# Kernel optimization log

Hardware: AMD Instinct MI355X
Metric: run time of the kernel (lower is better)

## Reference

```python
import jax, jax.numpy as jnp
import numpy as np
import math

NHEAD = 16
FACTOR = 5


def setup_inputs() -> dict:
    key = jax.random.key(0)
    ks = jax.random.split(key, 10)
    B, L, Dm = 2, 2048, 1024
    x = jax.random.normal(ks[0], (B, L, Dm), dtype=jnp.float32)
    w = lambda k: jax.random.normal(k, (Dm, Dm), dtype=jnp.float32) * 0.02
    b = lambda k: jax.random.normal(k, (Dm,), dtype=jnp.float32) * 0.02
    return {
        "x": x,
        "Wq": w(ks[1]), "bq": b(ks[2]),
        "Wk": w(ks[3]), "bk": b(ks[4]),
        "Wv": w(ks[5]), "bv": b(ks[6]),
        "Wo": w(ks[7]), "bo": b(ks[8]),
    }


def reference(x, Wq, bq, Wk, bk, Wv, bv, Wo, bo):
    B, L, Dm = x.shape
    H = NHEAD
    D = Dm // H
    # U = number of top scores kept per query row (ProbSparse sparsity level)
    U = min(L, int(FACTOR * math.log(L)) if L > 1 else L)

    def proj(W, b):
        # torch Linear: x @ W^T + b ; then [B,L,H,D] -> [B,H,L,D]
        return (x @ W.T + b).reshape(B, L, H, D).transpose(0, 2, 1, 3)

    Q = proj(Wq, bq)
    K = proj(Wk, bk)
    V = proj(Wv, bv)

    scores = jnp.einsum("bhqd,bhkd->bhqk", Q, K) / math.sqrt(D)  # [B,H,L,L]
    # kth-largest score per row; keep entries >= threshold (ties kept, matching torch semantics)
    thresh = jax.lax.top_k(scores, U)[0][..., -1:]  # [B,H,L,1]
    scores = jnp.where(scores < thresh, -jnp.inf, scores)
    attn = jax.nn.softmax(scores, axis=-1)  # dropout is identity in eval
    context = jnp.einsum("bhqk,bhkd->bhqd", attn, V)
    context = context.transpose(0, 2, 1, 3).reshape(B, L, Dm)
    return context @ Wo.T + bo
```

## Files before the change

### kernel.cpp

```cpp
#include <hip/hip_runtime.h>
#include <math.h>

#define BB 2
#define LL 2048
#define DM 1024
#define NH 16
#define HD 64

__device__ __forceinline__ unsigned mono32(float f) {
    unsigned u = __float_as_uint(f);
    return (u & 0x80000000u) ? ~u : (u | 0x80000000u);
}
__device__ __forceinline__ float unmono32(unsigned m) {
    const unsigned u = (m & 0x80000000u) ? (m & 0x7FFFFFFFu) : ~m;
    return __uint_as_float(u);
}

__global__ __launch_bounds__(256) void transpose1024(
    const float* __restrict__ in, float* __restrict__ out)
{
    __shared__ float t[32][33];
    const int bx = blockIdx.x * 32, by = blockIdx.y * 32;
    const int tx = threadIdx.x & 31, ty = threadIdx.x >> 5;
    for (int r = ty; r < 32; r += 8)
        t[r][tx] = in[(size_t)(by + r) * DM + bx + tx];
    __syncthreads();
    for (int r = ty; r < 32; r += 8)
        out[(size_t)(bx + r) * DM + by + tx] = t[tx][r];
}

__global__ __launch_bounds__(256) void proj_emul(
    const float* __restrict__ x, const float* __restrict__ Wt,
    const float* __restrict__ bias, float* __restrict__ outp)
{
    __shared__ float xs[8][DM];
    const int tid = threadIdx.x;
    const int n4  = tid * 4;
    const int m0  = blockIdx.x * 8;

    for (int i = tid; i < 8 * 256; i += 256) {
        const int r = i >> 8, c4 = (i & 255) << 2;
        *(float4*)&xs[r][c4] = *(const float4*)&x[(size_t)(m0 + r) * DM + c4];
    }
    __syncthreads();

    const int kbound[4] = {0, 384, 704, 1024};

    float S[8][4] = {};
#pragma unroll
    for (int p = 0; p < 3; p++) {
        float P[8][4] = {};
        for (int k = kbound[p]; k < kbound[p + 1]; k += 4) {
            const float4 w0 = *(const float4*)&Wt[(size_t)(k + 0) * DM + n4];
            const float4 w1 = *(const float4*)&Wt[(size_t)(k + 1) * DM + n4];
            const float4 w2 = *(const float4*)&Wt[(size_t)(k + 2) * DM + n4];
            const float4 w3 = *(const float4*)&Wt[(size_t)(k + 3) * DM + n4];
#pragma unroll
            for (int m = 0; m < 8; m++) {
                const float4 xv = *(const float4*)&xs[m][k];
                P[m][0] = fmaf(xv.x, w0.x, P[m][0]);
                P[m][1] = fmaf(xv.x, w0.y, P[m][1]);
                P[m][2] = fmaf(xv.x, w0.z, P[m][2]);
                P[m][3] = fmaf(xv.x, w0.w, P[m][3]);
                P[m][0] = fmaf(xv.y, w1.x, P[m][0]);
                P[m][1] = fmaf(xv.y, w1.y, P[m][1]);
                P[m][2] = fmaf(xv.y, w1.z, P[m][2]);
                P[m][3] = fmaf(xv.y, w1.w, P[m][3]);
                P[m][0] = fmaf(xv.z, w2.x, P[m][0]);
                P[m][1] = fmaf(xv.z, w2.y, P[m][1]);
                P[m][2] = fmaf(xv.z, w2.z, P[m][2]);
                P[m][3] = fmaf(xv.z, w2.w, P[m][3]);
                P[m][0] = fmaf(xv.w, w3.x, P[m][0]);
                P[m][1] = fmaf(xv.w, w3.y, P[m][1]);
                P[m][2] = fmaf(xv.w, w3.z, P[m][2]);
                P[m][3] = fmaf(xv.w, w3.w, P[m][3]);
            }
        }
#pragma unroll
        for (int m = 0; m < 8; m++) {
#pragma unroll
            for (int j = 0; j < 4; j++) S[m][j] += P[m][j];
        }
    }

    const float4 b4v = *(const float4*)&bias[n4];
    const int h = n4 / HD, d0 = n4 % HD;
#pragma unroll
    for (int m = 0; m < 8; m++) {
        const int mm = m0 + m;
        const int b = mm / LL, l = mm % LL;
        float4 o;
        o.x = S[m][0] + b4v.x; o.y = S[m][1] + b4v.y;
        o.z = S[m][2] + b4v.z; o.w = S[m][3] + b4v.w;
        *(float4*)&outp[(((size_t)b * NH + h) * LL + l) * HD + d0] = o;
    }
}

template <int MODE>
__global__ __launch_bounds__(256) void gemm_f32(
    const float* __restrict__ A, const float* __restrict__ W,
    const float* __restrict__ bias, float* __restrict__ out,
    int M, int N, int K)
{
    __shared__ float As[16][64];
    __shared__ float Bs[16][64];
    const int tid = threadIdx.x;
    const int m0 = blockIdx.y * 64;
    const int n0 = blockIdx.x * 64;
    const int tx = tid & 15, ty = tid >> 4;
    const int lr = tid >> 2, lc = (tid & 3) * 4;

    float acc[4][4] = {};

    for (int k0 = 0; k0 < K; k0 += 16) {
        float4 a4 = *(const float4*)&A[(size_t)(m0 + lr) * K + k0 + lc];
        float4 b4 = *(const float4*)&W[(size_t)(n0 + lr) * K + k0 + lc];
        __syncthreads();
        As[lc + 0][lr] = a4.x; As[lc + 1][lr] = a4.y;
        As[lc + 2][lr] = a4.z; As[lc + 3][lr] = a4.w;
        Bs[lc + 0][lr] = b4.x; Bs[lc + 1][lr] = b4.y;
        Bs[lc + 2][lr] = b4.z; Bs[lc + 3][lr] = b4.w;
        __syncthreads();
#pragma unroll
        for (int kk = 0; kk < 16; kk++) {
            float4 av = *(const float4*)&As[kk][ty * 4];
            float4 bv = *(const float4*)&Bs[kk][tx * 4];
            float a[4] = {av.x, av.y, av.z, av.w};
            float b[4] = {bv.x, bv.y, bv.z, bv.w};
#pragma unroll
            for (int i = 0; i < 4; i++)
#pragma unroll
                for (int j = 0; j < 4; j++)
                    acc[i][j] = fmaf(a[i], b[j], acc[i][j]);
        }
    }

#pragma unroll
    for (int i = 0; i < 4; i++) {
        const int m = m0 + ty * 4 + i;
#pragma unroll
        for (int j = 0; j < 4; j++) {
            const int n = n0 + tx * 4 + j;
            const float v = acc[i][j] + bias[n];
            if (MODE == 0) {
                const int b = m / LL, l = m % LL;
                const int h = n / HD, d = n % HD;
                out[(((size_t)b * NH + h) * LL + l) * HD + d] = v;
            } else {
                out[(size_t)m * N + n] = v;
            }
        }
    }
}

__global__ __launch_bounds__(256) void score_np(
    const float* __restrict__ Qf, const float* __restrict__ Kf,
    unsigned* __restrict__ scw, int bh0)
{
#pragma clang fp contract(off)
    const int tid  = threadIdx.x;
    const int lane = tid & 63;
    const int wv   = tid >> 6;
    const int l0   = blockIdx.x * 16;
    const int bhl  = blockIdx.y;
    const int bh   = bh0 + bhl;

    __shared__ float kt[256][68];
    __shared__ float qsh[16][64];

    const float* __restrict__ Kb = Kf + (size_t)bh * LL * HD;

    {
        const int r = tid >> 4, d4q = tid & 15;
        *(float4*)&qsh[r][d4q * 4] =
            *(const float4*)&Qf[((size_t)bh * LL + l0 + r) * HD + d4q * 4];
    }

    const int r0 = wv * 4;
    unsigned* __restrict__ s0 = scw + ((size_t)bhl * LL + l0 + r0 + 0) * LL;
    unsigned* __restrict__ s1 = scw + ((size_t)bhl * LL + l0 + r0 + 1) * LL;
    unsigned* __restrict__ s2 = scw + ((size_t)bhl * LL + l0 + r0 + 2) * LL;
    unsigned* __restrict__ s3 = scw + ((size_t)bhl * LL + l0 + r0 + 3) * LL;

    for (int kp = 0; kp < 8; kp++) {
        __syncthreads();
        {
            const float* src = Kb + ((size_t)kp * 256 + tid) * HD;
#pragma unroll
            for (int i = 0; i < 16; i++)
                *(float4*)&kt[tid][i * 4] = *(const float4*)&src[i * 4];
        }
        __syncthreads();

        float4 acc[4][4];
#pragma unroll
        for (int r = 0; r < 4; r++)
#pragma unroll
            for (int j = 0; j < 4; j++)
                acc[r][j] = make_float4(0.f, 0.f, 0.f, 0.f);

#pragma unroll
        for (int t = 0; t < 4; t++) {
#pragma unroll
            for (int sub = 3; sub >= 0; sub--) {
                const int d4 = 4 * t + sub;
                float4 kf0 = *(const float4*)&kt[0 * 64 + lane][d4 * 4];
                float4 kf1 = *(const float4*)&kt[1 * 64 + lane][d4 * 4];
                float4 kf2 = *(const float4*)&kt[2 * 64 + lane][d4 * 4];
                float4 kf3 = *(const float4*)&kt[3 * 64 + lane][d4 * 4];
                float4 qv0 = *(const float4*)&qsh[r0 + 0][d4 * 4];
                float4 qv1 = *(const float4*)&qsh[r0 + 1][d4 * 4];
                float4 qv2 = *(const float4*)&qsh[r0 + 2][d4 * 4];
                float4 qv3 = *(const float4*)&qsh[r0 + 3][d4 * 4];
#pragma unroll
                for (int r = 0; r < 4; r++) {
                    const float4 q = (r == 0) ? qv0 : (r == 1) ? qv1
                                   : (r == 2) ? qv2 : qv3;
#pragma unroll
                    for (int j = 0; j < 4; j++) {
                        const float4 k = (j == 0) ? kf0 : (j == 1) ? kf1
                                       : (j == 2) ? kf2 : kf3;
                        acc[r][j].x = q.x * k.x + acc[r][j].x;
                        acc[r][j].y = q.y * k.y + acc[r][j].y;
                        acc[r][j].z = q.z * k.z + acc[r][j].z;
                        acc[r][j].w = q.w * k.w + acc[r][j].w;
                    }
                }
            }
        }

#pragma unroll
        for (int j = 0; j < 4; j++) {
            const int kk = kp * 256 + j * 64 + lane;
            s0[kk] = mono32(((acc[0][j].x + acc[0][j].y) +
                             (acc[0][j].z + acc[0][j].w)) * 0.125f);
            s1[kk] = mono32(((acc[1][j].x + acc[1][j].y) +
                             (acc[1][j].z + acc[1][j].w)) * 0.125f);
            s2[kk] = mono32(((acc[2][j].x + acc[2][j].y) +
                             (acc[2][j].z + acc[2][j].w)) * 0.125f);
            s3[kk] = mono32(((acc[3][j].x + acc[3][j].y) +
                             (acc[3][j].z + acc[3][j].w)) * 0.125f);
        }
    }
}

__global__ __launch_bounds__(256) void select_np(
    const unsigned* __restrict__ scw, const float* __restrict__ Vf,
    float* __restrict__ ctx, int U, int bh0)
{
#pragma clang fp contract(off)
    const int tid  = threadIdx.x;
    const int lane = tid & 63;
    const int wv   = tid >> 6;
    const int l0   = blockIdx.x * 8;
    const int bhl  = blockIdx.y;
    const int bh   = bh0 + bhl;
    const int b    = bh / NH;
    const int h    = bh % NH;

    __shared__ float wls[8][64];
    __shared__ int   kls[8][64];

    const unsigned long long laneLT = (1ull << lane) - 1ull;
    const float* __restrict__ Vb = Vf + (size_t)bh * LL * HD;

#pragma unroll
    for (int rr8 = 0; rr8 < 2; rr8++) {
        const int rr = wv * 2 + rr8;
        const unsigned* __restrict__ srow =
            scw + ((size_t)bhl * LL + l0 + rr) * LL;

        unsigned mv[32];
#pragma unroll
        for (int j = 0; j < 32; j++) mv[j] = srow[lane + 64 * j];

        unsigned lo = 0u, hi = 0xFFFFFFFFu;
        while (lo < hi) {
            const unsigned span = hi - lo;
            const unsigned mid = lo + (span >> 1) + (span & 1u);
            int c = 0;
#pragma unroll
            for (int j = 0; j < 32; j++)
                c += (int)__popcll(__ballot(mv[j] >= mid));
            if (c >= U) lo = mid; else hi = mid - 1u;
        }

        unsigned mk = 0;
#pragma unroll
        for (int j = 0; j < 32; j++)
            if (mv[j] >= lo) mk = (mv[j] > mk) ? mv[j] : mk;
#pragma unroll
        for (int off = 32; off > 0; off >>= 1) {
            const unsigned o = __shfl_xor(mk, off, 64);
            mk = (o > mk) ? o : mk;
        }
        const float mx = unmono32(mk);

        int n = 0;
#pragma unroll
        for (int j = 0; j < 32; j++) {
            const bool p = (mv[j] >= lo);
            const unsigned long long ball = __ballot(p);
            if (p) {
                const int pos = n + (int)__popcll(ball & laneLT);
                if (pos < 64) {
                    kls[rr][pos] = lane + 64 * j;
                    wls[rr][pos] = expf(unmono32(mv[j]) - mx);
                }
            }
            n += (int)__popcll(ball);
        }
        if (n > 64) n = 64;

        float dl = (lane < n) ? wls[rr][lane] : 0.0f;
#pragma unroll
        for (int off = 32; off > 0; off >>= 1) dl += __shfl_xor(dl, off, 64);
        const float rden = 1.0f / dl;

        float acc = 0.0f;
        for (int c = 0; c < n; c++)
            acc = fmaf(wls[rr][c], Vb[(size_t)kls[rr][c] * HD + lane], acc);

        ctx[((size_t)b * LL + l0 + rr) * DM + h * HD + lane] = acc * rden;
    }
}

extern "C" void kernel_launch(void* const* d_in, const int* in_sizes, int n_in,
                              void* d_out, int out_size, void* d_ws, size_t ws_size,
                              hipStream_t stream)
{
    const float* x  = (const float*)d_in[0];
    const float* Wq = (const float*)d_in[1];
    const float* bq = (const float*)d_in[2];
    const float* Wk = (const float*)d_in[3];
    const float* bk = (const float*)d_in[4];
    const float* Wv = (const float*)d_in[5];
    const float* bv = (const float*)d_in[6];
    const float* Wo = (const float*)d_in[7];
    const float* bo = (const float*)d_in[8];
    float* out = (float*)d_out;

    const size_t E = (size_t)BB * NH * LL * HD;
    float* Wt1 = (float*)d_ws;
    float* Wt2 = Wt1 + (size_t)DM * DM;
    float* Qf  = Wt2 + (size_t)DM * DM;
    float* Kf  = Qf + E;
    float* Vf  = Kf + E;
    float* ctx = Vf + E;
    unsigned* scw = (unsigned*)(ctx + E);

    int U = (int)(5.0 * log((double)LL));
    if (U > LL) U = LL;

    const size_t base_bytes = (size_t)72 * 1024 * 1024;
    const size_t per_bh = (size_t)LL * LL * 4;
    size_t avail = (ws_size > base_bytes) ? (ws_size - base_bytes) : 0;
    int chunk = (int)(avail / per_bh);
    if (chunk < 1) chunk = 1;
    if (chunk > 8) chunk = 8;

    const int M = BB * LL;
    dim3 blk(256);
    dim3 gT(DM / 32, DM / 32);
    dim3 gP(M / 8);
    dim3 g64(DM / 64, M / 64);

    hipLaunchKernelGGL(transpose1024, gT, blk, 0, stream, Wq, Wt1);
    hipLaunchKernelGGL(transpose1024, gT, blk, 0, stream, Wk, Wt2);
    hipLaunchKernelGGL(proj_emul, gP, blk, 0, stream, x, Wt1, bq, Qf);
    hipLaunchKernelGGL(proj_emul, gP, blk, 0, stream, x, Wt2, bk, Kf);
    hipLaunchKernelGGL((gemm_f32<0>), g64, blk, 0, stream, x, Wv, bv, Vf, M, DM, DM);

    for (int bh0 = 0; bh0 < BB * NH; bh0 += chunk) {
        int nb = BB * NH - bh0;
        if (nb > chunk) nb = chunk;
        dim3 gA(LL / 16, nb);
        dim3 gS(LL / 8, nb);
        hipLaunchKernelGGL(score_np,  gA, blk, 0, stream, Qf, Kf, scw, bh0);
        hipLaunchKernelGGL(select_np, gS, blk, 0, stream, scw, Vf, ctx, U, bh0);
    }

    hipLaunchKernelGGL((gemm_f32<1>), g64, blk, 0, stream, ctx, Wo, bo, out, M, DM, DM);
}
```

Measured before the change: 1.995 ms.

## Halve score K tile and prefetch next tile into registers during compute

The score kernel now stages 128 keys per iteration instead of 256 and issues the global loads for the next tile into registers before computing the current one, writing them to shared memory after the math. Global load latency is meant to overlap with the FMA work, and the smaller LDS footprint may allow more blocks per CU. In exchange each thread holds 8 extra float4 registers, does fewer keys per iteration (2 instead of 4 K columns per lane), and runs twice as many barrier pairs.

```diff
diff --git a/kernel.cpp b/kernel.cpp
--- a/kernel.cpp
+++ b/kernel.cpp
@@ -165,7 +165,7 @@
     const int bhl  = blockIdx.y;
     const int bh   = bh0 + bhl;
 
-    __shared__ float kt[256][68];
+    __shared__ float kt[128][68];
     __shared__ float qsh[16][64];
 
     const float* __restrict__ Kb = Kf + (size_t)bh * LL * HD;
@@ -175,6 +175,13 @@
         *(float4*)&qsh[r][d4q * 4] =
             *(const float4*)&Qf[((size_t)bh * LL + l0 + r) * HD + d4q * 4];
     }
+#pragma unroll
+    for (int i = 0; i < 8; i++) {
+        const int idx = i * 256 + tid;
+        *(float4*)&kt[idx >> 4][(idx & 15) * 4] =
+            *(const float4*)&Kb[(size_t)(idx >> 4) * HD + (idx & 15) * 4];
+    }
+    __syncthreads();
 
     const int r0 = wv * 4;
     unsigned* __restrict__ s0 = scw + ((size_t)bhl * LL + l0 + r0 + 0) * LL;
@@ -182,64 +189,71 @@
     unsigned* __restrict__ s2 = scw + ((size_t)bhl * LL + l0 + r0 + 2) * LL;
     unsigned* __restrict__ s3 = scw + ((size_t)bhl * LL + l0 + r0 + 3) * LL;
 
-    for (int kp = 0; kp < 8; kp++) {
-        __syncthreads();
-        {
-            const float* src = Kb + ((size_t)kp * 256 + tid) * HD;
-#pragma unroll
-            for (int i = 0; i < 16; i++)
-                *(float4*)&kt[tid][i * 4] = *(const float4*)&src[i * 4];
-        }
-        __syncthreads();
-
-        float4 acc[4][4];
-#pragma unroll
-        for (int r = 0; r < 4; r++)
-#pragma unroll
-            for (int j = 0; j < 4; j++)
-                acc[r][j] = make_float4(0.f, 0.f, 0.f, 0.f);
-
+    for (int kp = 0; kp < 16; kp++) {
+        float4 pf[8];
+        if (kp < 15) {
+            const float* src = Kb + (size_t)(kp + 1) * 128 * HD;
+#pragma unroll
+            for (int i = 0; i < 8; i++) {
+                const int idx = i * 256 + tid;
+                pf[i] = *(const float4*)&src[(size_t)(idx >> 4) * HD +
+                                             (idx & 15) * 4];
+            }
+        }
+
+        float4 a00 = {0,0,0,0}, a01 = {0,0,0,0};
+        float4 a10 = {0,0,0,0}, a11 = {0,0,0,0};
+        float4 a20 = {0,0,0,0}, a21 = {0,0,0,0};
+        float4 a30 = {0,0,0,0}, a31 = {0,0,0,0};
 #pragma unroll
         for (int t = 0; t < 4; t++) {
 #pragma unroll
             for (int sub = 3; sub >= 0; sub--) {
                 const int d4 = 4 * t + sub;
-                float4 kf0 = *(const float4*)&kt[0 * 64 + lane][d4 * 4];
-                float4 kf1 = *(const float4*)&kt[1 * 64 + lane][d4 * 4];
-                float4 kf2 = *(const float4*)&kt[2 * 64 + lane][d4 * 4];
-                float4 kf3 = *(const float4*)&kt[3 * 64 + lane][d4 * 4];
-                float4 qv0 = *(const float4*)&qsh[r0 + 0][d4 * 4];
-                float4 qv1 = *(const float4*)&qsh[r0 + 1][d4 * 4];
-                float4 qv2 = *(const float4*)&qsh[r0 + 2][d4 * 4];
-                float4 qv3 = *(const float4*)&qsh[r0 + 3][d4 * 4];
-#pragma unroll
-                for (int r = 0; r < 4; r++) {
-                    const float4 q = (r == 0) ? qv0 : (r == 1) ? qv1
-                                   : (r == 2) ? qv2 : qv3;
-#pragma unroll
-                    for (int j = 0; j < 4; j++) {
-                        const float4 k = (j == 0) ? kf0 : (j == 1) ? kf1
-                                       : (j == 2) ? kf2 : kf3;
-                        acc[r][j].x = q.x * k.x + acc[r][j].x;
-                        acc[r][j].y = q.y * k.y + acc[r][j].y;
-                        acc[r][j].z = q.z * k.z + acc[r][j].z;
-                        acc[r][j].w = q.w * k.w + acc[r][j].w;
-                    }
-                }
-            }
-        }
-
-#pragma unroll
-        for (int j = 0; j < 4; j++) {
-            const int kk = kp * 256 + j * 64 + lane;
-            s0[kk] = mono32(((acc[0][j].x + acc[0][j].y) +
-                             (acc[0][j].z + acc[0][j].w)) * 0.125f);
-            s1[kk] = mono32(((acc[1][j].x + acc[1][j].y) +
-                             (acc[1][j].z + acc[1][j].w)) * 0.125f);
-            s2[kk] = mono32(((acc[2][j].x + acc[2][j].y) +
-                             (acc[2][j].z + acc[2][j].w)) * 0.125f);
-            s3[kk] = mono32(((acc[3][j].x + acc[3][j].y) +
-                             (acc[3][j].z + acc[3][j].w)) * 0.125f);
+                const float4 k0 = *(const float4*)&kt[0 * 64 + lane][d4 * 4];
+                const float4 k1 = *(const float4*)&kt[1 * 64 + lane][d4 * 4];
+                const float4 q0 = *(const float4*)&qsh[r0 + 0][d4 * 4];
+                const float4 q1 = *(const float4*)&qsh[r0 + 1][d4 * 4];
+                const float4 q2 = *(const float4*)&qsh[r0 + 2][d4 * 4];
+                const float4 q3 = *(const float4*)&qsh[r0 + 3][d4 * 4];
+                a00.x = q0.x * k0.x + a00.x; a00.y = q0.y * k0.y + a00.y;
+                a00.z = q0.z * k0.z + a00.z; a00.w = q0.w * k0.w + a00.w;
+                a01.x = q0.x * k1.x + a01.x; a01.y = q0.y * k1.y + a01.y;
+                a01.z = q0.z * k1.z + a01.z; a01.w = q0.w * k1.w + a01.w;
+                a10.x = q1.x * k0.x + a10.x; a10.y = q1.y * k0.y + a10.y;
+                a10.z = q1.z * k0.z + a10.z; a10.w = q1.w * k0.w + a10.w;
+                a11.x = q1.x * k1.x + a11.x; a11.y = q1.y * k1.y + a11.y;
+                a11.z = q1.z * k1.z + a11.z; a11.w = q1.w * k1.w + a11.w;
+                a20.x = q2.x * k0.x + a20.x; a20.y = q2.y * k0.y + a20.y;
+                a20.z = q2.z * k0.z + a20.z; a20.w = q2.w * k0.w + a20.w;
+                a21.x = q2.x * k1.x + a21.x; a21.y = q2.y * k1.y + a21.y;
+                a21.z = q2.z * k1.z + a21.z; a21.w = q2.w * k1.w + a21.w;
+                a30.x = q3.x * k0.x + a30.x; a30.y = q3.y * k0.y + a30.y;
+                a30.z = q3.z * k0.z + a30.z; a30.w = q3.w * k0.w + a30.w;
+                a31.x = q3.x * k1.x + a31.x; a31.y = q3.y * k1.y + a31.y;
+                a31.z = q3.z * k1.z + a31.z; a31.w = q3.w * k1.w + a31.w;
+            }
+        }
+
+        const int kkA = kp * 128 + lane;
+        const int kkB = kp * 128 + 64 + lane;
+        s0[kkA] = mono32(((a00.x + a00.y) + (a00.z + a00.w)) * 0.125f);
+        s0[kkB] = mono32(((a01.x + a01.y) + (a01.z + a01.w)) * 0.125f);
+        s1[kkA] = mono32(((a10.x + a10.y) + (a10.z + a10.w)) * 0.125f);
+        s1[kkB] = mono32(((a11.x + a11.y) + (a11.z + a11.w)) * 0.125f);
+        s2[kkA] = mono32(((a20.x + a20.y) + (a20.z + a20.w)) * 0.125f);
+        s2[kkB] = mono32(((a21.x + a21.y) + (a21.z + a21.w)) * 0.125f);
+        s3[kkA] = mono32(((a30.x + a30.y) + (a30.z + a30.w)) * 0.125f);
+        s3[kkB] = mono32(((a31.x + a31.y) + (a31.z + a31.w)) * 0.125f);
+
+        if (kp < 15) {
+            __syncthreads();
+#pragma unroll
+            for (int i = 0; i < 8; i++) {
+                const int idx = i * 256 + tid;
+                *(float4*)&kt[idx >> 4][(idx & 15) * 4] = pf[i];
+            }
+            __syncthreads();
         }
     }
 }
```

Measured after the change: 1.868 ms. 1.07x faster.
